# Performance work log

Hardware: AMD Instinct MI355X
Metric: run time of the kernel (lower is better)

The kernel has to match this reference:

```python
import jax, jax.numpy as jnp
import numpy as np

V = 32000   # num_tokens
D = 1024    # dim
L = 4       # depth
H = 8       # heads
B = 2       # batch
T = 2048    # seq_len (divisible by H)
SCALE = (D // H) ** -0.5  # scale uses dim//heads as in source
EPS = 1e-5
NEG_SLOPE = 0.01  # LeakyReLU default


def layernorm(x, g, b):
    mu = jnp.mean(x, axis=-1, keepdims=True)
    var = jnp.mean(jnp.square(x - mu), axis=-1, keepdims=True)
    return (x - mu) * jax.lax.rsqrt(var + EPS) * g + b


def setup_inputs() -> dict:
    key = jax.random.key(0)
    ks = jax.random.split(key, 8)
    s = 0.02
    f = lambda k, shape: jax.random.normal(k, shape, jnp.float32) * s
    return {
        "x": jax.random.randint(ks[0], (B, T), 0, V),
        "token_emb": f(ks[1], (V, D)),
        "ln1_g": jnp.ones((L, D), jnp.float32), "ln1_b": jnp.zeros((L, D), jnp.float32),
        "wqkv": f(ks[2], (L, D, 3 * D)),
        "wout_w": f(ks[3], (L, D, D)), "wout_b": jnp.zeros((L, D), jnp.float32),
        "ln2_g": jnp.ones((L, D), jnp.float32), "ln2_b": jnp.zeros((L, D), jnp.float32),
        "ff1_w": f(ks[4], (L, D, 4 * D)), "ff1_b": jnp.zeros((L, 4 * D), jnp.float32),
        "ff2_w": f(ks[5], (L, 4 * D, D)), "ff2_b": jnp.zeros((L, D), jnp.float32),
        "logit_w": f(ks[6], (D, V)), "logit_b": jnp.zeros((V,), jnp.float32),
    }


def reference(x, token_emb, ln1_g, ln1_b, wqkv, wout_w, wout_b,
              ln2_g, ln2_b, ff1_w, ff1_b, ff2_w, ff2_b, logit_w, logit_b):
    h = token_emb[x]  # [B, T, D]
    for i in range(L):
        # --- Residual(PreNorm(SelfAttention)) ---
        y = layernorm(h, ln1_g[i], ln1_b[i])
        qkv = y @ wqkv[i]                      # [B, T, 3D]
        q, k, v = jnp.split(qkv, 3, axis=-1)
        # faithful to source: reshape(b, -1, h, e) with e = full dim -> heads
        # partition the sequence into H strided groups, head-dim = D
        rs = lambda t: t.reshape(B, T // H, H, D).transpose(0, 2, 1, 3)  # [B, H, T/H, D]
        q, k, v = rs(q), rs(k), rs(v)
        dots = jnp.einsum('bhid,bhjd->bhij', q, k) * SCALE
        attn = jax.nn.softmax(dots, axis=-1)
        o = jnp.einsum('bhij,bhjd->bhid', attn, v)
        o = o.transpose(0, 2, 1, 3).reshape(B, T, D)
        h = h + (o @ wout_w[i] + wout_b[i])
        # --- Residual(PreNorm(FeedForward)) ---
        y = layernorm(h, ln2_g[i], ln2_b[i])
        y = y @ ff1_w[i] + ff1_b[i]
        y = jnp.where(y >= 0, y, NEG_SLOPE * y)  # LeakyReLU
        h = h + (y @ ff2_w[i] + ff2_b[i])
    return h @ logit_w + logit_b  # [B, T, V]
```

## Files before the change

### kernel.cpp

```cpp
#include <hip/hip_runtime.h>

#define DD 1024
#define LL 4
#define HH 8
#define BB 2
#define TT 2048
#define VV 32000
#define SCALE_QK 0.08838834764831845f

typedef __bf16 bf16x8 __attribute__((ext_vector_type(8)));
typedef __bf16 bf16x4 __attribute__((ext_vector_type(4)));
typedef float  f32x4  __attribute__((ext_vector_type(4)));

__device__ __forceinline__ void gload_lds16(const void* g, void* l) {
  __builtin_amdgcn_global_load_lds((const __attribute__((address_space(1))) void*)g,
                                   (__attribute__((address_space(3))) void*)l, 16, 0, 0);
}

template<int MODE>
__global__ __launch_bounds__(256, 2)
void gemm_mt(const __bf16* __restrict__ A, long ldA, long aSB, long aSH,
             const __bf16* __restrict__ Bt, long ldB, long bSB, long bSH,
             void* __restrict__ Cv, long ldC, long cSB, long cSH,
             const float* __restrict__ bias,
             const float* __restrict__ res, long ldR,
             int K)
{
  extern __shared__ __attribute__((aligned(16))) char smem[];

  int zbh = blockIdx.z;
  int kc = 0;
  if (MODE == 5) { kc = zbh >> 4; zbh &= 15; }
  if (MODE == 7) { kc = zbh; zbh = 0; }
  if (MODE == 5 || MODE == 7) {
    A  += (size_t)kc * K;
    Bt += (size_t)kc * K;
  }
  const int zb = zbh >> 3, zh = zbh & 7;
  A  += (size_t)zb * aSB + (size_t)zh * aSH;
  Bt += (size_t)zb * bSB + (size_t)zh * bSH;
  const size_t cOff = (MODE == 7) ? (size_t)kc * cSB
                                  : (size_t)zb * cSB + (size_t)zh * cSH;

  const int nbx = gridDim.x, nby = gridDim.y;
  const int nwg = nbx * nby;
  const int fid = blockIdx.y * nbx + blockIdx.x;
  const int q8 = nwg >> 3, r8 = nwg & 7;
  const int xcd = fid & 7, idx = fid >> 3;
  const int swz = (xcd < r8 ? xcd * (q8 + 1) : r8 * (q8 + 1) + (xcd - r8) * q8) + idx;
  int bx, by;
  if ((nby & 1) == 0) {
    const int W = 2 * nbx;
    const int grp = swz / W, t = swz - grp * W;
    bx = t >> 1; by = grp * 2 + (t & 1);
  } else {
    bx = swz / nby; by = swz - bx * nby;
  }
  const int m0 = by * 256, n0 = bx * 128;

  const int tid = threadIdx.x;
  const int wv = tid >> 6, ln = tid & 63;
  const int wm = wv >> 1, wn = wv & 1;

  const int usA = (ln & 7) ^ (ln >> 3);
  const int rsA = wv * 64 + 2 * (ln >> 3) + (usA >> 2);
  const int ksA = (usA & 3) * 8;
  const __bf16* pA0 = A + (size_t)(m0 + rsA) * ldA + ksA;
  const int usB = (tid & 7) ^ ((tid >> 3) & 7);
  const int rsB = 2 * (tid >> 3) + (usB >> 2);
  const int ksB = (usB & 3) * 8;
  const __bf16* pB0 = Bt + (size_t)(n0 + rsB) * ldB + ksB;

  const int lr = ln & 15;
  const int gfr = ((((ln & 1) << 2) | ((ln >> 4) & 3)) ^ ((ln >> 1) & 7)) << 4;
  const int aR = (wm * 64 + (lr >> 1)) * 128 + gfr;
  const int bR = 49152 + (wn * 32 + (lr >> 1)) * 128 + gfr;

  f32x4 acc[8][4] = {};
  const int NT = K >> 5;

#define STG(sl) { \
    char* da = smem + (sl) * 16384 + wv * 4096 + ln * 16; \
    gload_lds16(pA0,            da); \
    gload_lds16(pA0 + 16 * ldA, da + 1024); \
    gload_lds16(pA0 + 32 * ldA, da + 2048); \
    gload_lds16(pA0 + 48 * ldA, da + 3072); \
    char* db = smem + 49152 + (sl) * 8192 + tid * 16; \
    gload_lds16(pB0,            db); \
    gload_lds16(pB0 + 64 * ldB, db + 4096); \
    pA0 += 32; pB0 += 32; }

  STG(0);
  if (NT > 1) {
    STG(1);
    asm volatile("s_waitcnt vmcnt(6)" ::: "memory");
  } else {
    asm volatile("s_waitcnt vmcnt(0)" ::: "memory");
  }
  __builtin_amdgcn_s_barrier();

  int sc = 0, sn = 1, sf = 2;
  for (int t = 0; t < NT; ++t) {
    if (t + 2 < NT) STG(sf);
    const char* aBase = smem + sc * 16384 + aR;
    const char* bBase = smem + sc * 8192 + bR;
    bf16x8 a[8], b[4];
#pragma unroll
    for (int j = 0; j < 4; j++) b[j] = *(const bf16x8*)(bBase + j * 1024);
#pragma unroll
    for (int i = 0; i < 8; i++) a[i] = *(const bf16x8*)(aBase + i * 1024);
    __builtin_amdgcn_s_setprio(1);
#pragma unroll
    for (int i = 0; i < 8; i++)
#pragma unroll
      for (int j = 0; j < 4; j++)
        acc[i][j] = __builtin_amdgcn_mfma_f32_16x16x32_bf16(a[i], b[j], acc[i][j], 0, 0, 0);
    __builtin_amdgcn_s_setprio(0);
    if (t + 1 < NT) {
      if (t + 2 < NT) { asm volatile("s_waitcnt vmcnt(6)" ::: "memory"); }
      else            { asm volatile("s_waitcnt vmcnt(0)" ::: "memory"); }
      __builtin_amdgcn_sched_barrier(0);
      __builtin_amdgcn_s_barrier();
    }
    const int tmp = sc; sc = sn; sn = sf; sf = tmp;
  }
#undef STG

  const int rb = m0 + wm * 128 + (ln >> 4) * 4;
  const int cb = n0 + wn * 64 + lr;
#pragma unroll
  for (int i = 0; i < 8; i++)
#pragma unroll
    for (int j = 0; j < 4; j++) {
      const int col = cb + j * 16;
#pragma unroll
      for (int r = 0; r < 4; r++) {
        const int row = rb + i * 16 + r;
        float v = acc[i][j][r];
        const size_t ci = cOff + (size_t)row * ldC + col;
        if (MODE == 0)      ((__bf16*)Cv)[ci] = (__bf16)v;
        else if (MODE == 1) ((float*)Cv)[ci] = v;
        else if (MODE == 2) ((float*)Cv)[ci] = v + bias[col] + res[(size_t)row * ldR + col];
        else if (MODE == 3) { v += bias[col]; ((__bf16*)Cv)[ci] = (__bf16)(v >= 0.f ? v : 0.01f * v); }
        else if (MODE == 4) ((float*)Cv)[ci] = v + bias[col];
        else if (MODE == 5) atomicAdd(&((float*)Cv)[ci], v);
        else if (MODE == 7) ((float*)Cv)[ci] = v;
      }
    }
}

__global__ void wtrans(const float* __restrict__ W, __bf16* __restrict__ Wt, int K, int N)
{
  const size_t zo = (size_t)blockIdx.z * K * N;
  __shared__ float t[32][33];
  const int n0 = blockIdx.x * 32, k0 = blockIdx.y * 32;
  const int tx = threadIdx.x, ty = threadIdx.y;
#pragma unroll
  for (int r = 0; r < 4; r++)
    t[ty + r * 8][tx] = W[zo + (size_t)(k0 + ty + r * 8) * N + n0 + tx];
  __syncthreads();
#pragma unroll
  for (int r = 0; r < 4; r++)
    Wt[zo + (size_t)(n0 + ty + r * 8) * K + k0 + tx] = (__bf16)t[tx][ty + r * 8];
}

__global__ void vtrans(const __bf16* __restrict__ qkv, __bf16* __restrict__ Vt)
{
  const int z = blockIdx.z, bb = z >> 3, hh = z & 7;
  const __bf16* src = qkv + ((size_t)bb * TT + hh) * (3 * DD) + 2 * DD;
  __bf16* dst = Vt + (size_t)z * DD * 256;
  __shared__ __bf16 t[32][33];
  const int n0 = blockIdx.x * 32, i0 = blockIdx.y * 32;
  const int tx = threadIdx.x, ty = threadIdx.y;
#pragma unroll
  for (int r = 0; r < 4; r++)
    t[ty + r * 8][tx] = src[(size_t)(i0 + ty + r * 8) * (HH * 3 * DD) + n0 + tx];
  __syncthreads();
#pragma unroll
  for (int r = 0; r < 4; r++)
    dst[(size_t)(n0 + ty + r * 8) * 256 + i0 + tx] = t[tx][ty + r * 8];
}

__global__ void embed_k(const int* __restrict__ x, const float* __restrict__ emb, float* __restrict__ h)
{
  const int row = blockIdx.x;
  const int tok = x[row];
  ((float4*)(h + (size_t)row * DD))[threadIdx.x] = ((const float4*)(emb + (size_t)tok * DD))[threadIdx.x];
}

__global__ void ln_rows(const float* __restrict__ x, const float* __restrict__ g,
                        const float* __restrict__ b, __bf16* __restrict__ y)
{
  const int row = blockIdx.x, t = threadIdx.x;
  const int wv = t >> 6, ln = t & 63;
  const float4 v = ((const float4*)(x + (size_t)row * DD))[t];
  float s  = v.x + v.y + v.z + v.w;
  float ss = v.x * v.x + v.y * v.y + v.z * v.z + v.w * v.w;
#pragma unroll
  for (int o = 32; o; o >>= 1) { s += __shfl_xor(s, o); ss += __shfl_xor(ss, o); }
  __shared__ float rs_[4], rss_[4];
  if (!ln) { rs_[wv] = s; rss_[wv] = ss; }
  __syncthreads();
  s  = rs_[0] + rs_[1] + rs_[2] + rs_[3];
  ss = rss_[0] + rss_[1] + rss_[2] + rss_[3];
  const float mu  = s * (1.0f / DD);
  const float var = ss * (1.0f / DD) - mu * mu;
  const float r   = rsqrtf(var + 1e-5f);
  const float4 gv = ((const float4*)g)[t];
  const float4 bv = ((const float4*)b)[t];
  bf16x4 o = { (__bf16)((v.x - mu) * r * gv.x + bv.x),
               (__bf16)((v.y - mu) * r * gv.y + bv.y),
               (__bf16)((v.z - mu) * r * gv.z + bv.z),
               (__bf16)((v.w - mu) * r * gv.w + bv.w) };
  ((bf16x4*)(y + (size_t)row * DD))[t] = o;
}

__global__ void ln_acc(float* __restrict__ h, const float* __restrict__ P, long pStride,
                       const float* __restrict__ bias2,
                       const float* __restrict__ g, const float* __restrict__ b,
                       __bf16* __restrict__ y)
{
  const int row = blockIdx.x, t = threadIdx.x;
  const int wv = t >> 6, ln = t & 63;
  float4 v = ((const float4*)(h + (size_t)row * DD))[t];
#pragma unroll
  for (int c = 0; c < 4; c++) {
    const float4 p = ((const float4*)(P + (size_t)c * pStride + (size_t)row * DD))[t];
    v.x += p.x; v.y += p.y; v.z += p.z; v.w += p.w;
  }
  const float4 b2 = ((const float4*)bias2)[t];
  v.x += b2.x; v.y += b2.y; v.z += b2.z; v.w += b2.w;
  ((float4*)(h + (size_t)row * DD))[t] = v;
  float s  = v.x + v.y + v.z + v.w;
  float ss = v.x * v.x + v.y * v.y + v.z * v.z + v.w * v.w;
#pragma unroll
  for (int o = 32; o; o >>= 1) { s += __shfl_xor(s, o); ss += __shfl_xor(ss, o); }
  __shared__ float rs_[4], rss_[4];
  if (!ln) { rs_[wv] = s; rss_[wv] = ss; }
  __syncthreads();
  s  = rs_[0] + rs_[1] + rs_[2] + rs_[3];
  ss = rss_[0] + rss_[1] + rss_[2] + rss_[3];
  const float mu  = s * (1.0f / DD);
  const float var = ss * (1.0f / DD) - mu * mu;
  const float r   = rsqrtf(var + 1e-5f);
  const float4 gv = ((const float4*)g)[t];
  const float4 bv = ((const float4*)b)[t];
  bf16x4 o = { (__bf16)((v.x - mu) * r * gv.x + bv.x),
               (__bf16)((v.y - mu) * r * gv.y + bv.y),
               (__bf16)((v.z - mu) * r * gv.z + bv.z),
               (__bf16)((v.w - mu) * r * gv.w + bv.w) };
  ((bf16x4*)(y + (size_t)row * DD))[t] = o;
}

__global__ void f2bf_acc(const float* __restrict__ h, const float* __restrict__ P, long pStride,
                         const float* __restrict__ bias2, __bf16* __restrict__ y)
{
  const int row = blockIdx.x, t = threadIdx.x;
  float4 v = ((const float4*)(h + (size_t)row * DD))[t];
#pragma unroll
  for (int c = 0; c < 4; c++) {
    const float4 p = ((const float4*)(P + (size_t)c * pStride + (size_t)row * DD))[t];
    v.x += p.x; v.y += p.y; v.z += p.z; v.w += p.w;
  }
  const float4 b2 = ((const float4*)bias2)[t];
  bf16x4 o = { (__bf16)(v.x + b2.x), (__bf16)(v.y + b2.y),
               (__bf16)(v.z + b2.z), (__bf16)(v.w + b2.w) };
  ((bf16x4*)(y + (size_t)row * DD))[t] = o;
}

__global__ void softmax256(const float* __restrict__ S, __bf16* __restrict__ P)
{
  const int row = blockIdx.x, t = threadIdx.x;
  const int wv = t >> 6, ln = t & 63;
  const float v = S[(size_t)row * 256 + t] * SCALE_QK;
  float m = v;
#pragma unroll
  for (int o = 32; o; o >>= 1) m = fmaxf(m, __shfl_xor(m, o));
  __shared__ float red[8];
  if (!ln) red[wv] = m;
  __syncthreads();
  m = fmaxf(fmaxf(red[0], red[1]), fmaxf(red[2], red[3]));
  const float e = __expf(v - m);
  float s = e;
#pragma unroll
  for (int o = 32; o; o >>= 1) s += __shfl_xor(s, o);
  if (!ln) red[4 + wv] = s;
  __syncthreads();
  s = red[4] + red[5] + red[6] + red[7];
  P[(size_t)row * 256 + t] = (__bf16)(e / s);
}

template<int MODE>
static void G(const __bf16* A, long ldA, long aSB, long aSH,
              const __bf16* Bt, long ldB, long bSB, long bSH,
              void* C, long ldC, long cSB, long cSH,
              const float* bias, const float* res, long ldR,
              int M, int N, int K, int Z, hipStream_t s)
{
  hipFuncSetAttribute((const void*)gemm_mt<MODE>,
                      hipFuncAttributeMaxDynamicSharedMemorySize, 73728);
  gemm_mt<MODE><<<dim3(N / 128, M / 256, Z), 256, 73728, s>>>(
      A, ldA, aSB, aSH, Bt, ldB, bSB, bSH, C, ldC, cSB, cSH, bias, res, ldR, K);
}

extern "C" void kernel_launch(void* const* d_in, const int* in_sizes, int n_in,
                              void* d_out, int out_size, void* d_ws, size_t ws_size,
                              hipStream_t stream)
{
  const int*   x       = (const int*)  d_in[0];
  const float* emb     = (const float*)d_in[1];
  const float* ln1_g   = (const float*)d_in[2];
  const float* ln1_b   = (const float*)d_in[3];
  const float* wqkv    = (const float*)d_in[4];
  const float* wout_w  = (const float*)d_in[5];
  const float* wout_b  = (const float*)d_in[6];
  const float* ln2_g   = (const float*)d_in[7];
  const float* ln2_b   = (const float*)d_in[8];
  const float* ff1_w   = (const float*)d_in[9];
  const float* ff1_b   = (const float*)d_in[10];
  const float* ff2_w   = (const float*)d_in[11];
  const float* ff2_b   = (const float*)d_in[12];
  const float* logit_w = (const float*)d_in[13];
  const float* logit_b = (const float*)d_in[14];
  float* out = (float*)d_out;

  const int M = BB * TT;

  char* w = (char*)d_ws;
  size_t off = 0;
  auto take = [&](size_t bytes) { void* p = w + off; off += (bytes + 255) & ~(size_t)255; return p; };
  __bf16* wqkvT = (__bf16*)take((size_t)LL * 3 * DD * DD * 2);
  __bf16* woutT = (__bf16*)take((size_t)LL * DD * DD * 2);
  __bf16* ff1T  = (__bf16*)take((size_t)LL * 4 * DD * DD * 2);
  __bf16* ff2T  = (__bf16*)take((size_t)LL * DD * 4 * DD * 2);
  __bf16* logT  = (__bf16*)take((size_t)VV * DD * 2);
  float*  h     = (float*) take((size_t)M * DD * 4);
  __bf16* ybf   = (__bf16*)take((size_t)M * DD * 2);
  __bf16* qkvbf = (__bf16*)take((size_t)M * 3 * DD * 2);
  float*  Smat  = (float*) take((size_t)BB * HH * 256 * 256 * 4);
  __bf16* Pbf   = (__bf16*)take((size_t)BB * HH * 256 * 256 * 2);
  __bf16* Vt    = (__bf16*)take((size_t)BB * HH * DD * 256 * 2);
  __bf16* Obf   = (__bf16*)take((size_t)M * DD * 2);
  __bf16* midbf = (__bf16*)take((size_t)M * 4 * DD * 2);
  float*  part  = (float*) take((size_t)4 * M * DD * 4);
  if (ws_size < off) return;

  const dim3 tb(32, 8);
  wtrans<<<dim3(3 * DD / 32, DD / 32, LL), tb, 0, stream>>>(wqkv,   wqkvT, DD, 3 * DD);
  wtrans<<<dim3(DD / 32,     DD / 32, LL), tb, 0, stream>>>(wout_w, woutT, DD, DD);
  wtrans<<<dim3(4 * DD / 32, DD / 32, LL), tb, 0, stream>>>(ff1_w,  ff1T,  DD, 4 * DD);
  wtrans<<<dim3(DD / 32, 4 * DD / 32, LL), tb, 0, stream>>>(ff2_w,  ff2T,  4 * DD, DD);
  wtrans<<<dim3(VV / 32,     DD / 32, 1),  tb, 0, stream>>>(logit_w, logT, DD, VV);

  embed_k<<<M, 256, 0, stream>>>(x, emb, h);

  for (int l = 0; l < LL; l++) {
    if (l == 0)
      ln_rows<<<M, 256, 0, stream>>>(h, ln1_g, ln1_b, ybf);
    else
      ln_acc<<<M, 256, 0, stream>>>(h, part, (long)M * DD, ff2_b + (size_t)(l - 1) * DD,
                                    ln1_g + (size_t)l * DD, ln1_b + (size_t)l * DD, ybf);
    G<0>(ybf, DD, 0, 0, wqkvT + (size_t)l * 3 * DD * DD, DD, 0, 0,
         qkvbf, 3 * DD, 0, 0, nullptr, nullptr, 0, M, 3 * DD, DD, 1, stream);
    hipMemsetAsync(Smat, 0, (size_t)BB * HH * 256 * 256 * 4, stream);
    G<5>(qkvbf, HH * 3 * DD, (long)TT * 3 * DD, 3 * DD,
         qkvbf + DD, HH * 3 * DD, (long)TT * 3 * DD, 3 * DD,
         Smat, 256, (long)HH * 256 * 256, 256 * 256,
         nullptr, nullptr, 0, 256, 256, DD / 4, 4 * BB * HH, stream);
    softmax256<<<BB * HH * 256, 256, 0, stream>>>(Smat, Pbf);
    vtrans<<<dim3(DD / 32, 256 / 32, BB * HH), tb, 0, stream>>>(qkvbf, Vt);
    G<0>(Pbf, 256, (long)HH * 256 * 256, 256 * 256,
         Vt, 256, (long)HH * DD * 256, (long)DD * 256,
         Obf, HH * DD, (long)TT * DD, DD,
         nullptr, nullptr, 0, 256, DD, 256, BB * HH, stream);
    G<2>(Obf, DD, 0, 0, woutT + (size_t)l * DD * DD, DD, 0, 0,
         h, DD, 0, 0, wout_b + (size_t)l * DD, h, DD, M, DD, DD, 1, stream);
    ln_rows<<<M, 256, 0, stream>>>(h, ln2_g + (size_t)l * DD, ln2_b + (size_t)l * DD, ybf);
    G<3>(ybf, DD, 0, 0, ff1T + (size_t)l * 4 * DD * DD, DD, 0, 0,
         midbf, 4 * DD, 0, 0, ff1_b + (size_t)l * 4 * DD, nullptr, 0, M, 4 * DD, DD, 1, stream);
    G<7>(midbf, 4 * DD, 0, 0, ff2T + (size_t)l * DD * 4 * DD, 4 * DD, 0, 0,
         part, DD, (long)M * DD, 0, nullptr, nullptr, 0, M, DD, DD, 4, stream);
  }

  f2bf_acc<<<M, 256, 0, stream>>>(h, part, (long)M * DD, ff2_b + (size_t)3 * DD, ybf);
  G<4>(ybf, DD, 0, 0, logT, DD, 0, 0,
       out, VV, 0, 0, logit_b, nullptr, 0, M, VV, DD, 1, stream);
}
```

Before: 1.301 ms.

## Add 128x128-tile GEMM kernel for small attention and out-projection GEMMs

Adds a second GEMM kernel (gemm_rt) with 128x128 output tiles, 4x4 MFMA fragments per wave, static 48KB LDS triple-buffering and launch bounds targeting 3 blocks per CU. It replaces the 256x128-tile kernel for the QK^T split-K, PV and output-projection GEMMs. Those GEMMs launch few blocks with the large tile and under-fill the GPU. The smaller tile gives more workgroups and better occupancy, at the cost of less data reuse per block.

```diff
diff --git a/kernel.cpp b/kernel.cpp
--- a/kernel.cpp
+++ b/kernel.cpp
@@ -30,12 +30,7 @@
 
   int zbh = blockIdx.z;
   int kc = 0;
-  if (MODE == 5) { kc = zbh >> 4; zbh &= 15; }
-  if (MODE == 7) { kc = zbh; zbh = 0; }
-  if (MODE == 5 || MODE == 7) {
-    A  += (size_t)kc * K;
-    Bt += (size_t)kc * K;
-  }
+  if (MODE == 7) { kc = zbh; zbh = 0; A += (size_t)kc * K; Bt += (size_t)kc * K; }
   const int zb = zbh >> 3, zh = zbh & 7;
   A  += (size_t)zb * aSB + (size_t)zh * aSH;
   Bt += (size_t)zb * bSB + (size_t)zh * bSH;
@@ -139,12 +134,125 @@
         float v = acc[i][j][r];
         const size_t ci = cOff + (size_t)row * ldC + col;
         if (MODE == 0)      ((__bf16*)Cv)[ci] = (__bf16)v;
-        else if (MODE == 1) ((float*)Cv)[ci] = v;
         else if (MODE == 2) ((float*)Cv)[ci] = v + bias[col] + res[(size_t)row * ldR + col];
         else if (MODE == 3) { v += bias[col]; ((__bf16*)Cv)[ci] = (__bf16)(v >= 0.f ? v : 0.01f * v); }
         else if (MODE == 4) ((float*)Cv)[ci] = v + bias[col];
+        else if (MODE == 7) ((float*)Cv)[ci] = v;
+      }
+    }
+}
+
+template<int MODE>
+__global__ __launch_bounds__(256, 3)
+void gemm_rt(const __bf16* __restrict__ A, long ldA, long aSB, long aSH,
+             const __bf16* __restrict__ Bt, long ldB, long bSB, long bSH,
+             void* __restrict__ Cv, long ldC, long cSB, long cSH,
+             const float* __restrict__ bias,
+             const float* __restrict__ res, long ldR,
+             int K)
+{
+  int zbh = blockIdx.z;
+  if (MODE == 5) {
+    const int kc = zbh >> 4;
+    zbh &= 15;
+    A  += (size_t)kc * K;
+    Bt += (size_t)kc * K;
+  }
+  const int zb = zbh >> 3, zh = zbh & 7;
+  A  += (size_t)zb * aSB + (size_t)zh * aSH;
+  Bt += (size_t)zb * bSB + (size_t)zh * bSH;
+  const size_t cOff = (size_t)zb * cSB + (size_t)zh * cSH;
+
+  const int nbx = gridDim.x, nby = gridDim.y;
+  const int nwg = nbx * nby;
+  const int fid = blockIdx.y * nbx + blockIdx.x;
+  const int q8 = nwg >> 3, r8 = nwg & 7;
+  const int xcd = fid & 7, idx = fid >> 3;
+  const int swz = (xcd < r8 ? xcd * (q8 + 1) : r8 * (q8 + 1) + (xcd - r8) * q8) + idx;
+  const int bx = swz / nby, by = swz - bx * nby;
+  const int m0 = by * 128, n0 = bx * 128;
+
+  __shared__ __attribute__((aligned(16))) char smem[49152];
+
+  const int tid = threadIdx.x;
+  const int wv = tid >> 6, ln = tid & 63;
+  const int wm = wv >> 1, wn = wv & 1;
+
+  const int ls = tid >> 3;
+  const int gs = tid & 7;
+  const int us = gs ^ (ls & 7);
+  const int rs = 2 * ls + (us >> 2);
+  const int ks = (us & 3) * 8;
+  const __bf16* pA0 = A  + (size_t)(m0 + rs) * ldA + ks;
+  const __bf16* pA1 = A  + (size_t)(m0 + 64 + rs) * ldA + ks;
+  const __bf16* pB0 = Bt + (size_t)(n0 + rs) * ldB + ks;
+  const __bf16* pB1 = Bt + (size_t)(n0 + 64 + rs) * ldB + ks;
+
+  const int lr = ln & 15;
+  const int gfr = ((((ln & 1) << 2) | ((ln >> 4) & 3)) ^ ((ln >> 1) & 7)) << 4;
+  const int aR = (wm * 32 + (lr >> 1)) * 128 + gfr;
+  const int bR = 24576 + (wn * 32 + (lr >> 1)) * 128 + gfr;
+
+  f32x4 acc[4][4] = {};
+  const int NT = K >> 5;
+
+#define STG(sl) { \
+    char* da = smem + (sl) * 8192 + tid * 16; \
+    gload_lds16(pA0, da); gload_lds16(pA1, da + 4096); \
+    char* db = da + 24576; \
+    gload_lds16(pB0, db); gload_lds16(pB1, db + 4096); \
+    pA0 += 32; pA1 += 32; pB0 += 32; pB1 += 32; }
+
+  STG(0);
+  if (NT > 1) {
+    STG(1);
+    asm volatile("s_waitcnt vmcnt(4)" ::: "memory");
+  } else {
+    asm volatile("s_waitcnt vmcnt(0)" ::: "memory");
+  }
+  __builtin_amdgcn_s_barrier();
+
+  int sc = 0, sn = 1, sf = 2;
+  for (int t = 0; t < NT; ++t) {
+    if (t + 2 < NT) STG(sf);
+    const char* ba = smem + sc * 8192;
+    bf16x8 a[4], b[4];
+#pragma unroll
+    for (int i = 0; i < 4; i++) a[i] = *(const bf16x8*)(ba + aR + i * 1024);
+#pragma unroll
+    for (int j = 0; j < 4; j++) b[j] = *(const bf16x8*)(ba + bR + j * 1024);
+    __builtin_amdgcn_s_setprio(1);
+#pragma unroll
+    for (int i = 0; i < 4; i++)
+#pragma unroll
+      for (int j = 0; j < 4; j++)
+        acc[i][j] = __builtin_amdgcn_mfma_f32_16x16x32_bf16(a[i], b[j], acc[i][j], 0, 0, 0);
+    __builtin_amdgcn_s_setprio(0);
+    if (t + 1 < NT) {
+      if (t + 2 < NT) { asm volatile("s_waitcnt vmcnt(4)" ::: "memory"); }
+      else            { asm volatile("s_waitcnt vmcnt(0)" ::: "memory"); }
+      __builtin_amdgcn_sched_barrier(0);
+      __builtin_amdgcn_s_barrier();
+    }
+    const int tmp = sc; sc = sn; sn = sf; sf = tmp;
+  }
+#undef STG
+
+  const int rb = m0 + wm * 64 + (ln >> 4) * 4;
+  const int cb = n0 + wn * 64 + (ln & 15);
+#pragma unroll
+  for (int i = 0; i < 4; i++)
+#pragma unroll
+    for (int j = 0; j < 4; j++) {
+      const int col = cb + j * 16;
+#pragma unroll
+      for (int r = 0; r < 4; r++) {
+        const int row = rb + i * 16 + r;
+        float v = acc[i][j][r];
+        const size_t ci = cOff + (size_t)row * ldC + col;
+        if (MODE == 0)      ((__bf16*)Cv)[ci] = (__bf16)v;
+        else if (MODE == 2) ((float*)Cv)[ci] = v + bias[col] + res[(size_t)row * ldR + col];
         else if (MODE == 5) atomicAdd(&((float*)Cv)[ci], v);
-        else if (MODE == 7) ((float*)Cv)[ci] = v;
       }
     }
 }
@@ -300,6 +408,17 @@
   hipFuncSetAttribute((const void*)gemm_mt<MODE>,
                       hipFuncAttributeMaxDynamicSharedMemorySize, 73728);
   gemm_mt<MODE><<<dim3(N / 128, M / 256, Z), 256, 73728, s>>>(
+      A, ldA, aSB, aSH, Bt, ldB, bSB, bSH, C, ldC, cSB, cSH, bias, res, ldR, K);
+}
+
+template<int MODE>
+static void Gr(const __bf16* A, long ldA, long aSB, long aSH,
+               const __bf16* Bt, long ldB, long bSB, long bSH,
+               void* C, long ldC, long cSB, long cSH,
+               const float* bias, const float* res, long ldR,
+               int M, int N, int K, int Z, hipStream_t s)
+{
+  gemm_rt<MODE><<<dim3(N / 128, M / 128, Z), 256, 0, s>>>(
       A, ldA, aSB, aSH, Bt, ldB, bSB, bSH, C, ldC, cSB, cSH, bias, res, ldR, K);
 }
 
@@ -363,18 +482,18 @@
     G<0>(ybf, DD, 0, 0, wqkvT + (size_t)l * 3 * DD * DD, DD, 0, 0,
          qkvbf, 3 * DD, 0, 0, nullptr, nullptr, 0, M, 3 * DD, DD, 1, stream);
     hipMemsetAsync(Smat, 0, (size_t)BB * HH * 256 * 256 * 4, stream);
-    G<5>(qkvbf, HH * 3 * DD, (long)TT * 3 * DD, 3 * DD,
-         qkvbf + DD, HH * 3 * DD, (long)TT * 3 * DD, 3 * DD,
-         Smat, 256, (long)HH * 256 * 256, 256 * 256,
-         nullptr, nullptr, 0, 256, 256, DD / 4, 4 * BB * HH, stream);
+    Gr<5>(qkvbf, HH * 3 * DD, (long)TT * 3 * DD, 3 * DD,
+          qkvbf + DD, HH * 3 * DD, (long)TT * 3 * DD, 3 * DD,
+          Smat, 256, (long)HH * 256 * 256, 256 * 256,
+          nullptr, nullptr, 0, 256, 256, DD / 4, 4 * BB * HH, stream);
     softmax256<<<BB * HH * 256, 256, 0, stream>>>(Smat, Pbf);
     vtrans<<<dim3(DD / 32, 256 / 32, BB * HH), tb, 0, stream>>>(qkvbf, Vt);
-    G<0>(Pbf, 256, (long)HH * 256 * 256, 256 * 256,
-         Vt, 256, (long)HH * DD * 256, (long)DD * 256,
-         Obf, HH * DD, (long)TT * DD, DD,
-         nullptr, nullptr, 0, 256, DD, 256, BB * HH, stream);
-    G<2>(Obf, DD, 0, 0, woutT + (size_t)l * DD * DD, DD, 0, 0,
-         h, DD, 0, 0, wout_b + (size_t)l * DD, h, DD, M, DD, DD, 1, stream);
+    Gr<0>(Pbf, 256, (long)HH * 256 * 256, 256 * 256,
+          Vt, 256, (long)HH * DD * 256, (long)DD * 256,
+          Obf, HH * DD, (long)TT * DD, DD,
+          nullptr, nullptr, 0, 256, DD, 256, BB * HH, stream);
+    Gr<2>(Obf, DD, 0, 0, woutT + (size_t)l * DD * DD, DD, 0, 0,
+          h, DD, 0, 0, wout_b + (size_t)l * DD, h, DD, M, DD, DD, 1, stream);
     ln_rows<<<M, 256, 0, stream>>>(h, ln2_g + (size_t)l * DD, ln2_b + (size_t)l * DD, ybf);
     G<3>(ybf, DD, 0, 0, ff1T + (size_t)l * 4 * DD * DD, DD, 0, 0,
          midbf, 4 * DD, 0, 0, ff1_b + (size_t)l * 4 * DD, nullptr, 0, M, 4 * DD, DD, 1, stream);
```

Result: no change. 1.286 ms, median of 2 (-1.2%).
